# Kernel tuning notes

Hardware: AMD Instinct MI355X
Metric: run time of the kernel (lower is better)

The kernel has to match this reference:

```python
import jax, jax.numpy as jnp
import numpy as np

NEG_SLOPE = 0.2  # PyG GATConv default leaky_relu slope

N_NODES = 50000
N_EDGES = 800000
IN_DIM = 128
HID = 32
HEADS = 4


def setup_inputs() -> dict:
    key = jax.random.key(0)
    ks = jax.random.split(key, 12)
    x = jax.random.normal(ks[0], (N_NODES, IN_DIM), dtype=jnp.float32)
    edge_index = jax.random.randint(ks[1], (2, N_EDGES), 0, N_NODES, dtype=jnp.int64)
    s1 = 1.0 / np.sqrt(IN_DIM)
    s2 = 1.0 / np.sqrt(HID * HEADS)
    return {
        "x": x,
        "edge_index": edge_index,
        # layer 1: GATConv(IN_DIM -> HID, heads=HEADS, concat=True)
        "W1": jax.random.normal(ks[2], (IN_DIM, HEADS * HID), dtype=jnp.float32) * s1,
        "a_src1": jax.random.normal(ks[3], (HEADS, HID), dtype=jnp.float32) * s1,
        "a_dst1": jax.random.normal(ks[4], (HEADS, HID), dtype=jnp.float32) * s1,
        "b1": jnp.zeros((HEADS * HID,), dtype=jnp.float32),
        # head: GATConv(HEADS*HID -> 1, heads=1, concat=False)
        "W2": jax.random.normal(ks[5], (HEADS * HID, 1), dtype=jnp.float32) * s2,
        "a_src2": jax.random.normal(ks[6], (1, 1), dtype=jnp.float32) * s2,
        "a_dst2": jax.random.normal(ks[7], (1, 1), dtype=jnp.float32) * s2,
        "b2": jnp.zeros((1,), dtype=jnp.float32),
    }


def gat_conv(x, src, dst, W, a_src, a_dst, b, heads, out_ch, concat, n_nodes):
    # linear transform -> [N, H, C]
    h = (x @ W).reshape(n_nodes, heads, out_ch)
    # per-node attention halves -> [N, H]
    alpha_s = jnp.einsum('nhc,hc->nh', h, a_src)
    alpha_d = jnp.einsum('nhc,hc->nh', h, a_dst)
    # per-edge logits (gather), leaky relu -> [E, H]
    e = jax.nn.leaky_relu(alpha_s[src] + alpha_d[dst], NEG_SLOPE)
    # segment softmax over destination neighborhoods
    m = jax.ops.segment_max(e, dst, num_segments=n_nodes)  # [N, H]
    m = jnp.where(jnp.isfinite(m), m, 0.0)
    ex = jnp.exp(e - m[dst])
    denom = jax.ops.segment_sum(ex, dst, num_segments=n_nodes)  # [N, H]
    alpha = ex / (denom[dst] + 1e-16)  # [E, H]
    # weighted scatter-aggregate of source messages
    msg = h[src] * alpha[:, :, None]  # [E, H, C]
    out = jax.ops.segment_sum(msg, dst, num_segments=n_nodes)  # [N, H, C]
    out = out.reshape(n_nodes, heads * out_ch) if concat else out.mean(axis=1)
    return out + b


def reference(x, edge_index, W1, a_src1, a_dst1, b1, W2, a_src2, a_dst2, b2):
    n = x.shape[0]
    # PyG GATConv adds self-loops by default
    loops = jnp.arange(n, dtype=edge_index.dtype)
    src = jnp.concatenate([edge_index[0], loops])
    dst = jnp.concatenate([edge_index[1], loops])
    h = gat_conv(x, src, dst, W1, a_src1, a_dst1, b1, HEADS, HID, True, n)
    h = jax.nn.elu(h)  # dropout inactive in eval mode
    out = gat_conv(h, src, dst, W2, a_src2, a_dst2, b2, 1, 1, False, n)
    return out.squeeze(-1)  # [N]
```

## Files before the change

kernel.cpp:

```cpp
#include <hip/hip_runtime.h>
#include <hip/hip_bf16.h>
#include <hip/hip_fp16.h>

#define N_NODES 50000
#define N_EDGES 800000
#define E_TOT   850000
#define GBLK 64
#define GEMM_BLOCKS 782
#define NR 196
#define EPB 4096
#define BIN_BLOCKS 208
#define SEGCAP 8192

__global__ __launch_bounds__(512) void fat_kernel(const float* __restrict__ x,
                                                  const float* __restrict__ W1,
                                                  const float* __restrict__ asrc1,
                                                  const float* __restrict__ adst1,
                                                  __half* __restrict__ h1,
                                                  float* __restrict__ as1,
                                                  float* __restrict__ ad1,
                                                  const int* __restrict__ ei,
                                                  int* __restrict__ rangeCursor,
                                                  unsigned* __restrict__ gseg) {
    __shared__ float xs[32 * 65];
    __shared__ float sredA[8 * 64];
    __shared__ float sredB[8 * 64];
    __shared__ int cnt[NR];
    __shared__ int gbase[NR];

    const int tid = threadIdx.x;

    if (blockIdx.x < BIN_BLOCKS) {
        for (int i = tid; i < NR; i += 512) cnt[i] = 0;
        __syncthreads();

        int e0 = blockIdx.x * EPB + tid * 8;
        bool valid = (e0 < E_TOT);
        int src[8], dst[8], rg[8], rk[8];
        if (valid) {
            if (e0 < N_EDGES) {
                int4 a = *(const int4*)(ei + e0);
                int4 b = *(const int4*)(ei + e0 + 4);
                int4 c = *(const int4*)(ei + N_EDGES + e0);
                int4 d = *(const int4*)(ei + N_EDGES + e0 + 4);
                src[0]=a.x; src[1]=a.y; src[2]=a.z; src[3]=a.w;
                src[4]=b.x; src[5]=b.y; src[6]=b.z; src[7]=b.w;
                dst[0]=c.x; dst[1]=c.y; dst[2]=c.z; dst[3]=c.w;
                dst[4]=d.x; dst[5]=d.y; dst[6]=d.z; dst[7]=d.w;
            } else {
#pragma unroll
                for (int k = 0; k < 8; k++) { src[k] = dst[k] = e0 + k - N_EDGES; }
            }
#pragma unroll
            for (int k = 0; k < 8; k++) {
                rg[k] = dst[k] >> 8;
                rk[k] = atomicAdd(&cnt[rg[k]], 1);
            }
        }
        __syncthreads();
        for (int i = tid; i < NR; i += 512) {
            int c = cnt[i];
            gbase[i] = c ? atomicAdd(&rangeCursor[i], c) : 0;
        }
        __syncthreads();
        if (valid) {
#pragma unroll
            for (int k = 0; k < 8; k++) {
                int pos = gbase[rg[k]] + rk[k];
                if (pos < SEGCAP)
                    gseg[(size_t)rg[k] * SEGCAP + pos] =
                        ((unsigned)(dst[k] & 255) << 17) | (unsigned)src[k];
            }
        }
        return;
    }

    const int lane = tid & 63;
    const int w    = tid >> 6;
    const int head = __builtin_amdgcn_readfirstlane(w >> 1);
    const int ch   = __builtin_amdgcn_readfirstlane(w & 1);
    const int base = (blockIdx.x - BIN_BLOCKS) * GBLK;
    const int node = base + lane;

    const float* __restrict__ wh = W1 + head * 32 + ch * 16;

    float acc[16];
#pragma unroll
    for (int j = 0; j < 16; j++) acc[j] = 0.f;

    for (int kt = 0; kt < 4; kt++) {
        __syncthreads();
        {
            int row = tid >> 3, c4 = tid & 7;
            int n2 = base + row;
            float4 v = make_float4(0.f, 0.f, 0.f, 0.f);
            if (n2 < N_NODES)
                v = *(const float4*)(x + (size_t)n2 * 128 + kt * 32 + c4 * 4);
            xs[(c4 * 4 + 0) * 65 + row] = v.x;
            xs[(c4 * 4 + 1) * 65 + row] = v.y;
            xs[(c4 * 4 + 2) * 65 + row] = v.z;
            xs[(c4 * 4 + 3) * 65 + row] = v.w;
        }
        __syncthreads();

#pragma unroll 4
        for (int kk = 0; kk < 32; kk++) {
            float xv = xs[kk * 65 + lane];
            const float* __restrict__ wr = wh + (size_t)(kt * 32 + kk) * 128;
#pragma unroll
            for (int j = 0; j < 16; j++)
                acc[j] += xv * wr[j];
        }
    }

    if (node < N_NODES) {
        __half2 hp[8];
#pragma unroll
        for (int j = 0; j < 8; j++)
            hp[j] = __floats2half2_rn(acc[2 * j], acc[2 * j + 1]);
        float4* dst = (float4*)(h1 + (size_t)node * 128 + head * 32 + ch * 16);
        dst[0] = ((float4*)hp)[0];
        dst[1] = ((float4*)hp)[1];
    }

    float sa = 0.f, da = 0.f;
#pragma unroll
    for (int j = 0; j < 16; j++) {
        float v = acc[j];
        sa += v * asrc1[head * 32 + ch * 16 + j];
        da += v * adst1[head * 32 + ch * 16 + j];
    }
    sredA[w * 64 + lane] = sa;
    sredB[w * 64 + lane] = da;
    __syncthreads();
    if (tid < 256) {
        int hh = tid >> 6;
        int nd = base + lane;
        if (nd < N_NODES) {
            as1[nd * 4 + hh] = sredA[(hh * 2) * 64 + lane] + sredA[(hh * 2 + 1) * 64 + lane];
            ad1[nd * 4 + hh] = sredB[(hh * 2) * 64 + lane] + sredB[(hh * 2 + 1) * 64 + lane];
        }
    }
}

__global__ __launch_bounds__(512) void finalize_kernel(const int* __restrict__ rangeCursor,
                                                       const unsigned* __restrict__ gseg,
                                                       int* __restrict__ offs,
                                                       int* __restrict__ bucket) {
    __shared__ int rsc[256];
    __shared__ int cnt[256];
    __shared__ int csc[256];
    __shared__ int cur[256];
    __shared__ int lbuf[SEGCAP];

    const int tid = threadIdx.x;
    const int r = blockIdx.x;

    if (tid < 256) rsc[tid] = (tid < NR) ? min(rangeCursor[tid], SEGCAP) : 0;
    __syncthreads();
    for (int d = 1; d < 256; d <<= 1) {
        int u = (tid < 256 && tid >= d) ? rsc[tid - d] : 0;
        __syncthreads();
        if (tid < 256) rsc[tid] += u;
        __syncthreads();
    }
    const int n = min(rangeCursor[r], SEGCAP);
    const int rbase = rsc[r] - n;
    const unsigned* __restrict__ seg = gseg + (size_t)r * SEGCAP;

    if (tid < 256) cnt[tid] = 0;
    __syncthreads();
    for (int i = tid; i < n; i += 512)
        atomicAdd(&cnt[seg[i] >> 17], 1);
    __syncthreads();
    if (tid < 256) csc[tid] = cnt[tid];
    __syncthreads();
    for (int d = 1; d < 256; d <<= 1) {
        int u = (tid < 256 && tid >= d) ? csc[tid - d] : 0;
        __syncthreads();
        if (tid < 256) csc[tid] += u;
        __syncthreads();
    }
    if (tid < 256) {
        int lofs = csc[tid] - cnt[tid];
        cur[tid] = lofs;
        int node = r * 256 + tid;
        if (node < N_NODES) offs[node] = rbase + lofs;
    }
    if (r == NR - 1 && tid == 0) offs[N_NODES] = rbase + n;
    __syncthreads();
    for (int i = tid; i < n; i += 512) {
        unsigned en = seg[i];
        int p = atomicAdd(&cur[en >> 17], 1);
        lbuf[p] = (int)(en & 0x1FFFFu);
    }
    __syncthreads();
    for (int i = tid; i < n; i += 512)
        bucket[rbase + i] = lbuf[i];
}

__global__ __launch_bounds__(256) void agg1_kernel(const __half* __restrict__ h1,
                                                   const float* __restrict__ as1,
                                                   const float* __restrict__ ad1,
                                                   const int* __restrict__ offs,
                                                   const int* __restrict__ bucket,
                                                   const float* __restrict__ b1,
                                                   const float* __restrict__ W2,
                                                   float* __restrict__ h2s) {
    int w = threadIdx.x >> 6, l = threadIdx.x & 63;
    int node = blockIdx.x * 4 + w;
    if (node >= N_NODES) return;
    int sub = l & 15;
    int ep  = l >> 4;
    int head = sub >> 2;
    float adh = ad1[node * 4 + head];
    int a = offs[node];
    int deg = offs[node + 1] - a;

    float c[8];
#pragma unroll
    for (int k = 0; k < 8; k++) c[k] = 0.f;
    float sx = 0.f;

    for (int i = 0; i < deg; i += 4) {
        int idx = i + ep;
        bool valid = idx < deg;
        int s = bucket[a + (valid ? idx : 0)];
        float e = as1[s * 4 + head] + adh;
        e = fmaxf(e, 0.2f * e);
        float ex = valid ? __expf(e) : 0.f;
        float4 hv = *(const float4*)(h1 + (size_t)s * 128 + sub * 8);
        const __half2* hh = (const __half2*)&hv;
        float2 f0 = __half22float2(hh[0]);
        float2 f1 = __half22float2(hh[1]);
        float2 f2 = __half22float2(hh[2]);
        float2 f3 = __half22float2(hh[3]);
        sx += ex;
        c[0] += ex * f0.x; c[1] += ex * f0.y;
        c[2] += ex * f1.x; c[3] += ex * f1.y;
        c[4] += ex * f2.x; c[5] += ex * f2.y;
        c[6] += ex * f3.x; c[7] += ex * f3.y;
    }

#pragma unroll
    for (int k = 0; k < 8; k++) {
        c[k] += __shfl_xor(c[k], 16, 64);
        c[k] += __shfl_xor(c[k], 32, 64);
    }
    sx += __shfl_xor(sx, 16, 64);
    sx += __shfl_xor(sx, 32, 64);

    float r = 1.f / (sx + 1e-16f);
    float4 blo = ((const float4*)b1)[sub * 2];
    float4 bhi = ((const float4*)b1)[sub * 2 + 1];
    float4 wlo = ((const float4*)W2)[sub * 2];
    float4 whi = ((const float4*)W2)[sub * 2 + 1];
    float ob[8] = {blo.x, blo.y, blo.z, blo.w, bhi.x, bhi.y, bhi.z, bhi.w};
    float ow[8] = {wlo.x, wlo.y, wlo.z, wlo.w, whi.x, whi.y, whi.z, whi.w};
    float p = 0.f;
#pragma unroll
    for (int k = 0; k < 8; k++) {
        float o = c[k] * r + ob[k];
        float el = (o > 0.f) ? o : (__expf(o) - 1.f);
        p += el * ow[k];
    }
    p += __shfl_xor(p, 1, 64);
    p += __shfl_xor(p, 2, 64);
    p += __shfl_xor(p, 4, 64);
    p += __shfl_xor(p, 8, 64);
    if (l == 0) h2s[node] = p;
}

__global__ __launch_bounds__(256) void agg2_kernel(const float* __restrict__ h2s,
                                                   const int* __restrict__ offs,
                                                   const int* __restrict__ bucket,
                                                   const float* __restrict__ asrc2,
                                                   const float* __restrict__ adst2,
                                                   const float* __restrict__ b2,
                                                   float* __restrict__ out) {
    int w = threadIdx.x >> 6, l = threadIdx.x & 63;
    int node = blockIdx.x * 4 + w;
    if (node >= N_NODES) return;
    float asc = asrc2[0], adc = adst2[0], bias = b2[0];
    float adn = h2s[node] * adc;
    int a = offs[node], b = offs[node + 1];
    float sx = 0.f, sw = 0.f;
    for (int i = a + l; i < b; i += 64) {
        float hs = h2s[bucket[i]];
        float e = hs * asc + adn;
        e = fmaxf(e, 0.2f * e);
        float ex = __expf(e);
        sx += ex;
        sw += ex * hs;
    }
#pragma unroll
    for (int o = 32; o > 0; o >>= 1) {
        sx += __shfl_xor(sx, o, 64);
        sw += __shfl_xor(sw, o, 64);
    }
    if (l == 0) out[node] = sw / (sx + 1e-16f) + bias;
}


extern "C" void kernel_launch(void* const* d_in, const int* in_sizes, int n_in,
                              void* d_out, int out_size, void* d_ws, size_t ws_size,
                              hipStream_t stream) {
    const float* x     = (const float*)d_in[0];
    const int*   ei    = (const int*)d_in[1];
    const float* W1    = (const float*)d_in[2];
    const float* asrc1 = (const float*)d_in[3];
    const float* adst1 = (const float*)d_in[4];
    const float* b1    = (const float*)d_in[5];
    const float* W2    = (const float*)d_in[6];
    const float* asrc2 = (const float*)d_in[7];
    const float* adst2 = (const float*)d_in[8];
    const float* b2    = (const float*)d_in[9];
    float* out = (float*)d_out;

    char* ws = (char*)d_ws;
    size_t o = 0;
    auto alloc = [&](size_t bytes) -> void* {
        void* p = ws + o;
        o += (bytes + 255) & ~(size_t)255;
        return p;
    };
    int* offs    = (int*)alloc((size_t)(N_NODES + 1) * 4);
    int* bucket  = (int*)alloc((size_t)E_TOT * 4);
    __half* h1   = (__half*)alloc((size_t)N_NODES * 128 * 2);
    float* as1   = (float*)alloc((size_t)N_NODES * 4 * 4);
    float* ad1   = (float*)alloc((size_t)N_NODES * 4 * 4);
    float* h2s   = (float*)alloc((size_t)N_NODES * 4);
    int* rangeCursor = (int*)alloc((size_t)NR * 4);
    unsigned* gseg   = (unsigned*)alloc((size_t)NR * SEGCAP * 4);

    hipMemsetAsync(rangeCursor, 0, (size_t)NR * 4, stream);

    fat_kernel<<<BIN_BLOCKS + GEMM_BLOCKS, 512, 0, stream>>>(
        x, W1, asrc1, adst1, h1, as1, ad1, ei, rangeCursor, gseg);

    finalize_kernel<<<NR, 512, 0, stream>>>(rangeCursor, gseg, offs, bucket);

    agg1_kernel<<<(N_NODES + 3) / 4, 256, 0, stream>>>(
        h1, as1, ad1, offs, bucket, b1, W2, h2s);

    agg2_kernel<<<(N_NODES + 3) / 4, 256, 0, stream>>>(
        h2s, offs, bucket, asrc2, adst2, b2, out);
}
```

Baseline: 102.7 us.

## Move GEMM alongside CSR finalize and widen agg1 per-lane feature slice

The edge-binning pass now runs as its own kernel, and the CSR finalize blocks are merged with the layer-1 GEMM blocks into a single launch that shares a union shared-memory buffer. The GEMM then overlaps with the finalize step instead of with binning, which balances load across the two launches. Separately, agg1 now has each lane handle 16 channels with two float4 loads, so a wavefront processes 8 edges per iteration instead of 4. This doubles the accumulator registers and adds a shuffle stage in exchange for fewer, wider gathers. The merged kernel's shared memory becomes the larger finalize size (about 36KB), which may cut occupancy for the GEMM blocks.

```diff
diff --git a/kernel.cpp b/kernel.cpp
--- a/kernel.cpp
+++ b/kernel.cpp
@@ -12,74 +12,131 @@
 #define BIN_BLOCKS 208
 #define SEGCAP 8192
 
-__global__ __launch_bounds__(512) void fat_kernel(const float* __restrict__ x,
-                                                  const float* __restrict__ W1,
-                                                  const float* __restrict__ asrc1,
-                                                  const float* __restrict__ adst1,
-                                                  __half* __restrict__ h1,
-                                                  float* __restrict__ as1,
-                                                  float* __restrict__ ad1,
-                                                  const int* __restrict__ ei,
+__global__ __launch_bounds__(512) void bin_kernel(const int* __restrict__ ei,
                                                   int* __restrict__ rangeCursor,
                                                   unsigned* __restrict__ gseg) {
-    __shared__ float xs[32 * 65];
-    __shared__ float sredA[8 * 64];
-    __shared__ float sredB[8 * 64];
     __shared__ int cnt[NR];
     __shared__ int gbase[NR];
-
     const int tid = threadIdx.x;
 
-    if (blockIdx.x < BIN_BLOCKS) {
-        for (int i = tid; i < NR; i += 512) cnt[i] = 0;
-        __syncthreads();
-
-        int e0 = blockIdx.x * EPB + tid * 8;
-        bool valid = (e0 < E_TOT);
-        int src[8], dst[8], rg[8], rk[8];
-        if (valid) {
-            if (e0 < N_EDGES) {
-                int4 a = *(const int4*)(ei + e0);
-                int4 b = *(const int4*)(ei + e0 + 4);
-                int4 c = *(const int4*)(ei + N_EDGES + e0);
-                int4 d = *(const int4*)(ei + N_EDGES + e0 + 4);
-                src[0]=a.x; src[1]=a.y; src[2]=a.z; src[3]=a.w;
-                src[4]=b.x; src[5]=b.y; src[6]=b.z; src[7]=b.w;
-                dst[0]=c.x; dst[1]=c.y; dst[2]=c.z; dst[3]=c.w;
-                dst[4]=d.x; dst[5]=d.y; dst[6]=d.z; dst[7]=d.w;
-            } else {
-#pragma unroll
-                for (int k = 0; k < 8; k++) { src[k] = dst[k] = e0 + k - N_EDGES; }
-            }
-#pragma unroll
-            for (int k = 0; k < 8; k++) {
-                rg[k] = dst[k] >> 8;
-                rk[k] = atomicAdd(&cnt[rg[k]], 1);
-            }
-        }
-        __syncthreads();
-        for (int i = tid; i < NR; i += 512) {
-            int c = cnt[i];
-            gbase[i] = c ? atomicAdd(&rangeCursor[i], c) : 0;
-        }
-        __syncthreads();
-        if (valid) {
-#pragma unroll
-            for (int k = 0; k < 8; k++) {
-                int pos = gbase[rg[k]] + rk[k];
-                if (pos < SEGCAP)
-                    gseg[(size_t)rg[k] * SEGCAP + pos] =
-                        ((unsigned)(dst[k] & 255) << 17) | (unsigned)src[k];
-            }
-        }
+    for (int i = tid; i < NR; i += 512) cnt[i] = 0;
+    __syncthreads();
+
+    int e0 = blockIdx.x * EPB + tid * 8;
+    bool valid = (e0 < E_TOT);
+    int src[8], dst[8], rg[8], rk[8];
+    if (valid) {
+        if (e0 < N_EDGES) {
+            int4 a = *(const int4*)(ei + e0);
+            int4 b = *(const int4*)(ei + e0 + 4);
+            int4 c = *(const int4*)(ei + N_EDGES + e0);
+            int4 d = *(const int4*)(ei + N_EDGES + e0 + 4);
+            src[0]=a.x; src[1]=a.y; src[2]=a.z; src[3]=a.w;
+            src[4]=b.x; src[5]=b.y; src[6]=b.z; src[7]=b.w;
+            dst[0]=c.x; dst[1]=c.y; dst[2]=c.z; dst[3]=c.w;
+            dst[4]=d.x; dst[5]=d.y; dst[6]=d.z; dst[7]=d.w;
+        } else {
+#pragma unroll
+            for (int k = 0; k < 8; k++) { src[k] = dst[k] = e0 + k - N_EDGES; }
+        }
+#pragma unroll
+        for (int k = 0; k < 8; k++) {
+            rg[k] = dst[k] >> 8;
+            rk[k] = atomicAdd(&cnt[rg[k]], 1);
+        }
+    }
+    __syncthreads();
+    for (int i = tid; i < NR; i += 512) {
+        int c = cnt[i];
+        gbase[i] = c ? atomicAdd(&rangeCursor[i], c) : 0;
+    }
+    __syncthreads();
+    if (valid) {
+#pragma unroll
+        for (int k = 0; k < 8; k++) {
+            int pos = gbase[rg[k]] + rk[k];
+            if (pos < SEGCAP)
+                gseg[(size_t)rg[k] * SEGCAP + pos] =
+                    ((unsigned)(dst[k] & 255) << 17) | (unsigned)src[k];
+        }
+    }
+}
+
+__global__ __launch_bounds__(512) void fatgf_kernel(const int* __restrict__ rangeCursor,
+                                                    const unsigned* __restrict__ gseg,
+                                                    int* __restrict__ offs,
+                                                    int* __restrict__ bucket,
+                                                    const float* __restrict__ x,
+                                                    const float* __restrict__ W1,
+                                                    const float* __restrict__ asrc1,
+                                                    const float* __restrict__ adst1,
+                                                    __half* __restrict__ h1,
+                                                    float* __restrict__ as1,
+                                                    float* __restrict__ ad1) {
+    __shared__ __align__(16) char smem[(1024 + SEGCAP) * 4];
+    const int tid = threadIdx.x;
+
+    if (blockIdx.x < NR) {
+        int* rsc  = (int*)smem;
+        int* cnt  = rsc + 256;
+        int* csc  = cnt + 256;
+        int* cur  = csc + 256;
+        int* lbuf = cur + 256;
+        const int r = blockIdx.x;
+
+        if (tid < 256) rsc[tid] = (tid < NR) ? min(rangeCursor[tid], SEGCAP) : 0;
+        __syncthreads();
+        for (int d = 1; d < 256; d <<= 1) {
+            int u = (tid < 256 && tid >= d) ? rsc[tid - d] : 0;
+            __syncthreads();
+            if (tid < 256) rsc[tid] += u;
+            __syncthreads();
+        }
+        const int n = min(rangeCursor[r], SEGCAP);
+        const int rbase = rsc[r] - n;
+        const unsigned* __restrict__ seg = gseg + (size_t)r * SEGCAP;
+
+        if (tid < 256) cnt[tid] = 0;
+        __syncthreads();
+        for (int i = tid; i < n; i += 512)
+            atomicAdd(&cnt[seg[i] >> 17], 1);
+        __syncthreads();
+        if (tid < 256) csc[tid] = cnt[tid];
+        __syncthreads();
+        for (int d = 1; d < 256; d <<= 1) {
+            int u = (tid < 256 && tid >= d) ? csc[tid - d] : 0;
+            __syncthreads();
+            if (tid < 256) csc[tid] += u;
+            __syncthreads();
+        }
+        if (tid < 256) {
+            int lofs = csc[tid] - cnt[tid];
+            cur[tid] = lofs;
+            int node = r * 256 + tid;
+            if (node < N_NODES) offs[node] = rbase + lofs;
+        }
+        if (r == NR - 1 && tid == 0) offs[N_NODES] = rbase + n;
+        __syncthreads();
+        for (int i = tid; i < n; i += 512) {
+            unsigned en = seg[i];
+            int p = atomicAdd(&cur[en >> 17], 1);
+            lbuf[p] = (int)(en & 0x1FFFFu);
+        }
+        __syncthreads();
+        for (int i = tid; i < n; i += 512)
+            bucket[rbase + i] = lbuf[i];
         return;
     }
+
+    float* xs    = (float*)smem;
+    float* sredA = xs + 32 * 65;
+    float* sredB = sredA + 8 * 64;
 
     const int lane = tid & 63;
     const int w    = tid >> 6;
     const int head = __builtin_amdgcn_readfirstlane(w >> 1);
     const int ch   = __builtin_amdgcn_readfirstlane(w & 1);
-    const int base = (blockIdx.x - BIN_BLOCKS) * GBLK;
+    const int base = (blockIdx.x - NR) * GBLK;
     const int node = base + lane;
 
     const float* __restrict__ wh = W1 + head * 32 + ch * 16;
@@ -141,62 +198,6 @@
             ad1[nd * 4 + hh] = sredB[(hh * 2) * 64 + lane] + sredB[(hh * 2 + 1) * 64 + lane];
         }
     }
-}
-
-__global__ __launch_bounds__(512) void finalize_kernel(const int* __restrict__ rangeCursor,
-                                                       const unsigned* __restrict__ gseg,
-                                                       int* __restrict__ offs,
-                                                       int* __restrict__ bucket) {
-    __shared__ int rsc[256];
-    __shared__ int cnt[256];
-    __shared__ int csc[256];
-    __shared__ int cur[256];
-    __shared__ int lbuf[SEGCAP];
-
-    const int tid = threadIdx.x;
-    const int r = blockIdx.x;
-
-    if (tid < 256) rsc[tid] = (tid < NR) ? min(rangeCursor[tid], SEGCAP) : 0;
-    __syncthreads();
-    for (int d = 1; d < 256; d <<= 1) {
-        int u = (tid < 256 && tid >= d) ? rsc[tid - d] : 0;
-        __syncthreads();
-        if (tid < 256) rsc[tid] += u;
-        __syncthreads();
-    }
-    const int n = min(rangeCursor[r], SEGCAP);
-    const int rbase = rsc[r] - n;
-    const unsigned* __restrict__ seg = gseg + (size_t)r * SEGCAP;
-
-    if (tid < 256) cnt[tid] = 0;
-    __syncthreads();
-    for (int i = tid; i < n; i += 512)
-        atomicAdd(&cnt[seg[i] >> 17], 1);
-    __syncthreads();
-    if (tid < 256) csc[tid] = cnt[tid];
-    __syncthreads();
-    for (int d = 1; d < 256; d <<= 1) {
-        int u = (tid < 256 && tid >= d) ? csc[tid - d] : 0;
-        __syncthreads();
-        if (tid < 256) csc[tid] += u;
-        __syncthreads();
-    }
-    if (tid < 256) {
-        int lofs = csc[tid] - cnt[tid];
-        cur[tid] = lofs;
-        int node = r * 256 + tid;
-        if (node < N_NODES) offs[node] = rbase + lofs;
-    }
-    if (r == NR - 1 && tid == 0) offs[N_NODES] = rbase + n;
-    __syncthreads();
-    for (int i = tid; i < n; i += 512) {
-        unsigned en = seg[i];
-        int p = atomicAdd(&cur[en >> 17], 1);
-        lbuf[p] = (int)(en & 0x1FFFFu);
-    }
-    __syncthreads();
-    for (int i = tid; i < n; i += 512)
-        bucket[rbase + i] = lbuf[i];
 }
 
 __global__ __launch_bounds__(256) void agg1_kernel(const __half* __restrict__ h1,
@@ -210,64 +211,75 @@
     int w = threadIdx.x >> 6, l = threadIdx.x & 63;
     int node = blockIdx.x * 4 + w;
     if (node >= N_NODES) return;
-    int sub = l & 15;
-    int ep  = l >> 4;
-    int head = sub >> 2;
+    int sub = l & 7;
+    int ep  = l >> 3;
+    int head = sub >> 1;
     float adh = ad1[node * 4 + head];
     int a = offs[node];
     int deg = offs[node + 1] - a;
 
-    float c[8];
-#pragma unroll
-    for (int k = 0; k < 8; k++) c[k] = 0.f;
+    float c[16];
+#pragma unroll
+    for (int k = 0; k < 16; k++) c[k] = 0.f;
     float sx = 0.f;
 
-    for (int i = 0; i < deg; i += 4) {
+    for (int i = 0; i < deg; i += 8) {
         int idx = i + ep;
         bool valid = idx < deg;
         int s = bucket[a + (valid ? idx : 0)];
         float e = as1[s * 4 + head] + adh;
         e = fmaxf(e, 0.2f * e);
         float ex = valid ? __expf(e) : 0.f;
-        float4 hv = *(const float4*)(h1 + (size_t)s * 128 + sub * 8);
-        const __half2* hh = (const __half2*)&hv;
-        float2 f0 = __half22float2(hh[0]);
-        float2 f1 = __half22float2(hh[1]);
-        float2 f2 = __half22float2(hh[2]);
-        float2 f3 = __half22float2(hh[3]);
+        const float4* hp = (const float4*)(h1 + (size_t)s * 128 + sub * 16);
+        float4 hv0 = hp[0];
+        float4 hv1 = hp[1];
+        const __half2* h0 = (const __half2*)&hv0;
+        const __half2* h1p = (const __half2*)&hv1;
         sx += ex;
-        c[0] += ex * f0.x; c[1] += ex * f0.y;
-        c[2] += ex * f1.x; c[3] += ex * f1.y;
-        c[4] += ex * f2.x; c[5] += ex * f2.y;
-        c[6] += ex * f3.x; c[7] += ex * f3.y;
-    }
-
-#pragma unroll
-    for (int k = 0; k < 8; k++) {
+#pragma unroll
+        for (int q = 0; q < 4; q++) {
+            float2 f = __half22float2(h0[q]);
+            c[2 * q]     += ex * f.x;
+            c[2 * q + 1] += ex * f.y;
+        }
+#pragma unroll
+        for (int q = 0; q < 4; q++) {
+            float2 f = __half22float2(h1p[q]);
+            c[8 + 2 * q] += ex * f.x;
+            c[9 + 2 * q] += ex * f.y;
+        }
+    }
+
+#pragma unroll
+    for (int k = 0; k < 16; k++) {
+        c[k] += __shfl_xor(c[k], 8, 64);
         c[k] += __shfl_xor(c[k], 16, 64);
         c[k] += __shfl_xor(c[k], 32, 64);
     }
+    sx += __shfl_xor(sx, 8, 64);
     sx += __shfl_xor(sx, 16, 64);
     sx += __shfl_xor(sx, 32, 64);
 
     float r = 1.f / (sx + 1e-16f);
-    float4 blo = ((const float4*)b1)[sub * 2];
-    float4 bhi = ((const float4*)b1)[sub * 2 + 1];
-    float4 wlo = ((const float4*)W2)[sub * 2];
-    float4 whi = ((const float4*)W2)[sub * 2 + 1];
-    float ob[8] = {blo.x, blo.y, blo.z, blo.w, bhi.x, bhi.y, bhi.z, bhi.w};
-    float ow[8] = {wlo.x, wlo.y, wlo.z, wlo.w, whi.x, whi.y, whi.z, whi.w};
+    const float4* bp = (const float4*)(b1 + sub * 16);
+    const float4* wp = (const float4*)(W2 + sub * 16);
     float p = 0.f;
 #pragma unroll
-    for (int k = 0; k < 8; k++) {
-        float o = c[k] * r + ob[k];
-        float el = (o > 0.f) ? o : (__expf(o) - 1.f);
-        p += el * ow[k];
+    for (int q = 0; q < 4; q++) {
+        float4 bv = bp[q];
+        float4 wv = wp[q];
+        float ob[4] = {bv.x, bv.y, bv.z, bv.w};
+        float ow[4] = {wv.x, wv.y, wv.z, wv.w};
+#pragma unroll
+        for (int t = 0; t < 4; t++) {
+            float o = c[q * 4 + t] * r + ob[t];
+            float el = (o > 0.f) ? o : (__expf(o) - 1.f);
+            p += el * ow[t];
+        }
     }
     p += __shfl_xor(p, 1, 64);
     p += __shfl_xor(p, 2, 64);
     p += __shfl_xor(p, 4, 64);
-    p += __shfl_xor(p, 8, 64);
     if (l == 0) h2s[node] = p;
 }
 
@@ -335,10 +347,11 @@
 
     hipMemsetAsync(rangeCursor, 0, (size_t)NR * 4, stream);
 
-    fat_kernel<<<BIN_BLOCKS + GEMM_BLOCKS, 512, 0, stream>>>(
-        x, W1, asrc1, adst1, h1, as1, ad1, ei, rangeCursor, gseg);
-
-    finalize_kernel<<<NR, 512, 0, stream>>>(rangeCursor, gseg, offs, bucket);
+    bin_kernel<<<BIN_BLOCKS, 512, 0, stream>>>(ei, rangeCursor, gseg);
+
+    fatgf_kernel<<<NR + GEMM_BLOCKS, 512, 0, stream>>>(
+        rangeCursor, gseg, offs, bucket,
+        x, W1, asrc1, adst1, h1, as1, ad1);
 
     agg1_kernel<<<(N_NODES + 3) / 4, 256, 0, stream>>>(
         h1, as1, ad1, offs, bucket, b1, W2, h2s);
```

Result: no change. 103.7 us (+1.0%).

## Pair GEMM with CSR finalize and stage edge logits per wave in agg1

Applied to the files above, without the earlier changes.

The binning pass becomes its own kernel. The GEMM blocks now run alongside the CSR finalize blocks in one fused launch that reuses a shared-memory union, so the dense transform overlaps with the sort instead of with binning. agg1 now loads each chunk of 64 neighbour indices once per wave, computes all four heads' exp logits with one vector load, and stages them in LDS before the gather loop. This removes redundant bucket/as1 loads and exp work, at the cost of extra LDS traffic and a larger shared footprint in the fused kernel, which may lower occupancy of the GEMM blocks.

```diff
diff --git a/kernel.cpp b/kernel.cpp
--- a/kernel.cpp
+++ b/kernel.cpp
@@ -12,74 +12,131 @@
 #define BIN_BLOCKS 208
 #define SEGCAP 8192
 
-__global__ __launch_bounds__(512) void fat_kernel(const float* __restrict__ x,
-                                                  const float* __restrict__ W1,
-                                                  const float* __restrict__ asrc1,
-                                                  const float* __restrict__ adst1,
-                                                  __half* __restrict__ h1,
-                                                  float* __restrict__ as1,
-                                                  float* __restrict__ ad1,
-                                                  const int* __restrict__ ei,
+__global__ __launch_bounds__(512) void bin_kernel(const int* __restrict__ ei,
                                                   int* __restrict__ rangeCursor,
                                                   unsigned* __restrict__ gseg) {
-    __shared__ float xs[32 * 65];
-    __shared__ float sredA[8 * 64];
-    __shared__ float sredB[8 * 64];
     __shared__ int cnt[NR];
     __shared__ int gbase[NR];
-
     const int tid = threadIdx.x;
 
-    if (blockIdx.x < BIN_BLOCKS) {
-        for (int i = tid; i < NR; i += 512) cnt[i] = 0;
-        __syncthreads();
-
-        int e0 = blockIdx.x * EPB + tid * 8;
-        bool valid = (e0 < E_TOT);
-        int src[8], dst[8], rg[8], rk[8];
-        if (valid) {
-            if (e0 < N_EDGES) {
-                int4 a = *(const int4*)(ei + e0);
-                int4 b = *(const int4*)(ei + e0 + 4);
-                int4 c = *(const int4*)(ei + N_EDGES + e0);
-                int4 d = *(const int4*)(ei + N_EDGES + e0 + 4);
-                src[0]=a.x; src[1]=a.y; src[2]=a.z; src[3]=a.w;
-                src[4]=b.x; src[5]=b.y; src[6]=b.z; src[7]=b.w;
-                dst[0]=c.x; dst[1]=c.y; dst[2]=c.z; dst[3]=c.w;
-                dst[4]=d.x; dst[5]=d.y; dst[6]=d.z; dst[7]=d.w;
-            } else {
-#pragma unroll
-                for (int k = 0; k < 8; k++) { src[k] = dst[k] = e0 + k - N_EDGES; }
-            }
-#pragma unroll
-            for (int k = 0; k < 8; k++) {
-                rg[k] = dst[k] >> 8;
-                rk[k] = atomicAdd(&cnt[rg[k]], 1);
-            }
-        }
-        __syncthreads();
-        for (int i = tid; i < NR; i += 512) {
-            int c = cnt[i];
-            gbase[i] = c ? atomicAdd(&rangeCursor[i], c) : 0;
-        }
-        __syncthreads();
-        if (valid) {
-#pragma unroll
-            for (int k = 0; k < 8; k++) {
-                int pos = gbase[rg[k]] + rk[k];
-                if (pos < SEGCAP)
-                    gseg[(size_t)rg[k] * SEGCAP + pos] =
-                        ((unsigned)(dst[k] & 255) << 17) | (unsigned)src[k];
-            }
-        }
+    for (int i = tid; i < NR; i += 512) cnt[i] = 0;
+    __syncthreads();
+
+    int e0 = blockIdx.x * EPB + tid * 8;
+    bool valid = (e0 < E_TOT);
+    int src[8], dst[8], rg[8], rk[8];
+    if (valid) {
+        if (e0 < N_EDGES) {
+            int4 a = *(const int4*)(ei + e0);
+            int4 b = *(const int4*)(ei + e0 + 4);
+            int4 c = *(const int4*)(ei + N_EDGES + e0);
+            int4 d = *(const int4*)(ei + N_EDGES + e0 + 4);
+            src[0]=a.x; src[1]=a.y; src[2]=a.z; src[3]=a.w;
+            src[4]=b.x; src[5]=b.y; src[6]=b.z; src[7]=b.w;
+            dst[0]=c.x; dst[1]=c.y; dst[2]=c.z; dst[3]=c.w;
+            dst[4]=d.x; dst[5]=d.y; dst[6]=d.z; dst[7]=d.w;
+        } else {
+#pragma unroll
+            for (int k = 0; k < 8; k++) { src[k] = dst[k] = e0 + k - N_EDGES; }
+        }
+#pragma unroll
+        for (int k = 0; k < 8; k++) {
+            rg[k] = dst[k] >> 8;
+            rk[k] = atomicAdd(&cnt[rg[k]], 1);
+        }
+    }
+    __syncthreads();
+    for (int i = tid; i < NR; i += 512) {
+        int c = cnt[i];
+        gbase[i] = c ? atomicAdd(&rangeCursor[i], c) : 0;
+    }
+    __syncthreads();
+    if (valid) {
+#pragma unroll
+        for (int k = 0; k < 8; k++) {
+            int pos = gbase[rg[k]] + rk[k];
+            if (pos < SEGCAP)
+                gseg[(size_t)rg[k] * SEGCAP + pos] =
+                    ((unsigned)(dst[k] & 255) << 17) | (unsigned)src[k];
+        }
+    }
+}
+
+__global__ __launch_bounds__(512) void fatgf_kernel(const int* __restrict__ rangeCursor,
+                                                    const unsigned* __restrict__ gseg,
+                                                    int* __restrict__ offs,
+                                                    int* __restrict__ bucket,
+                                                    const float* __restrict__ x,
+                                                    const float* __restrict__ W1,
+                                                    const float* __restrict__ asrc1,
+                                                    const float* __restrict__ adst1,
+                                                    __half* __restrict__ h1,
+                                                    float* __restrict__ as1,
+                                                    float* __restrict__ ad1) {
+    __shared__ __align__(16) char smem[(1024 + SEGCAP) * 4];
+    const int tid = threadIdx.x;
+
+    if (blockIdx.x < NR) {
+        int* rsc  = (int*)smem;
+        int* cnt  = rsc + 256;
+        int* csc  = cnt + 256;
+        int* cur  = csc + 256;
+        int* lbuf = cur + 256;
+        const int r = blockIdx.x;
+
+        if (tid < 256) rsc[tid] = (tid < NR) ? min(rangeCursor[tid], SEGCAP) : 0;
+        __syncthreads();
+        for (int d = 1; d < 256; d <<= 1) {
+            int u = (tid < 256 && tid >= d) ? rsc[tid - d] : 0;
+            __syncthreads();
+            if (tid < 256) rsc[tid] += u;
+            __syncthreads();
+        }
+        const int n = min(rangeCursor[r], SEGCAP);
+        const int rbase = rsc[r] - n;
+        const unsigned* __restrict__ seg = gseg + (size_t)r * SEGCAP;
+
+        if (tid < 256) cnt[tid] = 0;
+        __syncthreads();
+        for (int i = tid; i < n; i += 512)
+            atomicAdd(&cnt[seg[i] >> 17], 1);
+        __syncthreads();
+        if (tid < 256) csc[tid] = cnt[tid];
+        __syncthreads();
+        for (int d = 1; d < 256; d <<= 1) {
+            int u = (tid < 256 && tid >= d) ? csc[tid - d] : 0;
+            __syncthreads();
+            if (tid < 256) csc[tid] += u;
+            __syncthreads();
+        }
+        if (tid < 256) {
+            int lofs = csc[tid] - cnt[tid];
+            cur[tid] = lofs;
+            int node = r * 256 + tid;
+            if (node < N_NODES) offs[node] = rbase + lofs;
+        }
+        if (r == NR - 1 && tid == 0) offs[N_NODES] = rbase + n;
+        __syncthreads();
+        for (int i = tid; i < n; i += 512) {
+            unsigned en = seg[i];
+            int p = atomicAdd(&cur[en >> 17], 1);
+            lbuf[p] = (int)(en & 0x1FFFFu);
+        }
+        __syncthreads();
+        for (int i = tid; i < n; i += 512)
+            bucket[rbase + i] = lbuf[i];
         return;
     }
+
+    float* xs    = (float*)smem;
+    float* sredA = xs + 32 * 65;
+    float* sredB = sredA + 8 * 64;
 
     const int lane = tid & 63;
     const int w    = tid >> 6;
     const int head = __builtin_amdgcn_readfirstlane(w >> 1);
     const int ch   = __builtin_amdgcn_readfirstlane(w & 1);
-    const int base = (blockIdx.x - BIN_BLOCKS) * GBLK;
+    const int base = (blockIdx.x - NR) * GBLK;
     const int node = base + lane;
 
     const float* __restrict__ wh = W1 + head * 32 + ch * 16;
@@ -143,62 +200,6 @@
     }
 }
 
-__global__ __launch_bounds__(512) void finalize_kernel(const int* __restrict__ rangeCursor,
-                                                       const unsigned* __restrict__ gseg,
-                                                       int* __restrict__ offs,
-                                                       int* __restrict__ bucket) {
-    __shared__ int rsc[256];
-    __shared__ int cnt[256];
-    __shared__ int csc[256];
-    __shared__ int cur[256];
-    __shared__ int lbuf[SEGCAP];
-
-    const int tid = threadIdx.x;
-    const int r = blockIdx.x;
-
-    if (tid < 256) rsc[tid] = (tid < NR) ? min(rangeCursor[tid], SEGCAP) : 0;
-    __syncthreads();
-    for (int d = 1; d < 256; d <<= 1) {
-        int u = (tid < 256 && tid >= d) ? rsc[tid - d] : 0;
-        __syncthreads();
-        if (tid < 256) rsc[tid] += u;
-        __syncthreads();
-    }
-    const int n = min(rangeCursor[r], SEGCAP);
-    const int rbase = rsc[r] - n;
-    const unsigned* __restrict__ seg = gseg + (size_t)r * SEGCAP;
-
-    if (tid < 256) cnt[tid] = 0;
-    __syncthreads();
-    for (int i = tid; i < n; i += 512)
-        atomicAdd(&cnt[seg[i] >> 17], 1);
-    __syncthreads();
-    if (tid < 256) csc[tid] = cnt[tid];
-    __syncthreads();
-    for (int d = 1; d < 256; d <<= 1) {
-        int u = (tid < 256 && tid >= d) ? csc[tid - d] : 0;
-        __syncthreads();
-        if (tid < 256) csc[tid] += u;
-        __syncthreads();
-    }
-    if (tid < 256) {
-        int lofs = csc[tid] - cnt[tid];
-        cur[tid] = lofs;
-        int node = r * 256 + tid;
-        if (node < N_NODES) offs[node] = rbase + lofs;
-    }
-    if (r == NR - 1 && tid == 0) offs[N_NODES] = rbase + n;
-    __syncthreads();
-    for (int i = tid; i < n; i += 512) {
-        unsigned en = seg[i];
-        int p = atomicAdd(&cur[en >> 17], 1);
-        lbuf[p] = (int)(en & 0x1FFFFu);
-    }
-    __syncthreads();
-    for (int i = tid; i < n; i += 512)
-        bucket[rbase + i] = lbuf[i];
-}
-
 __global__ __launch_bounds__(256) void agg1_kernel(const __half* __restrict__ h1,
                                                    const float* __restrict__ as1,
                                                    const float* __restrict__ ad1,
@@ -207,39 +208,65 @@
                                                    const float* __restrict__ b1,
                                                    const float* __restrict__ W2,
                                                    float* __restrict__ h2s) {
+    __shared__ int   sbuf[4][64];
+    __shared__ float exbuf[4][64][4];
+
     int w = threadIdx.x >> 6, l = threadIdx.x & 63;
     int node = blockIdx.x * 4 + w;
     if (node >= N_NODES) return;
     int sub = l & 15;
     int ep  = l >> 4;
     int head = sub >> 2;
-    float adh = ad1[node * 4 + head];
     int a = offs[node];
     int deg = offs[node + 1] - a;
+    float4 adv = *(const float4*)(ad1 + (size_t)node * 4);
 
     float c[8];
 #pragma unroll
     for (int k = 0; k < 8; k++) c[k] = 0.f;
     float sx = 0.f;
 
-    for (int i = 0; i < deg; i += 4) {
-        int idx = i + ep;
-        bool valid = idx < deg;
-        int s = bucket[a + (valid ? idx : 0)];
-        float e = as1[s * 4 + head] + adh;
-        e = fmaxf(e, 0.2f * e);
-        float ex = valid ? __expf(e) : 0.f;
-        float4 hv = *(const float4*)(h1 + (size_t)s * 128 + sub * 8);
-        const __half2* hh = (const __half2*)&hv;
-        float2 f0 = __half22float2(hh[0]);
-        float2 f1 = __half22float2(hh[1]);
-        float2 f2 = __half22float2(hh[2]);
-        float2 f3 = __half22float2(hh[3]);
-        sx += ex;
-        c[0] += ex * f0.x; c[1] += ex * f0.y;
-        c[2] += ex * f1.x; c[3] += ex * f1.y;
-        c[4] += ex * f2.x; c[5] += ex * f2.y;
-        c[6] += ex * f3.x; c[7] += ex * f3.y;
+    for (int base = 0; base < deg; base += 64) {
+        int cd = min(deg - base, 64);
+        {
+            bool v = l < cd;
+            int s = bucket[a + base + (v ? l : 0)];
+            sbuf[w][l] = s;
+            float4 asv = *(const float4*)(as1 + (size_t)s * 4);
+            float e0 = asv.x + adv.x, e1 = asv.y + adv.y;
+            float e2 = asv.z + adv.z, e3 = asv.w + adv.w;
+            e0 = fmaxf(e0, 0.2f * e0);
+            e1 = fmaxf(e1, 0.2f * e1);
+            e2 = fmaxf(e2, 0.2f * e2);
+            e3 = fmaxf(e3, 0.2f * e3);
+            float4 exv;
+            exv.x = v ? __expf(e0) : 0.f;
+            exv.y = v ? __expf(e1) : 0.f;
+            exv.z = v ? __expf(e2) : 0.f;
+            exv.w = v ? __expf(e3) : 0.f;
+            *(float4*)&exbuf[w][l][0] = exv;
+        }
+        __builtin_amdgcn_wave_barrier();
+        for (int g = 0; g < cd; g += 4) {
+            int j = g + ep;
+            bool v2 = j < cd;
+            int jj = v2 ? j : 0;
+            int s = sbuf[w][jj];
+            float ex = exbuf[w][jj][head];
+            if (!v2) ex = 0.f;
+            float4 hv = *(const float4*)(h1 + (size_t)s * 128 + sub * 8);
+            const __half2* hh = (const __half2*)&hv;
+            float2 f0 = __half22float2(hh[0]);
+            float2 f1 = __half22float2(hh[1]);
+            float2 f2 = __half22float2(hh[2]);
+            float2 f3 = __half22float2(hh[3]);
+            sx += ex;
+            c[0] += ex * f0.x; c[1] += ex * f0.y;
+            c[2] += ex * f1.x; c[3] += ex * f1.y;
+            c[4] += ex * f2.x; c[5] += ex * f2.y;
+            c[6] += ex * f3.x; c[7] += ex * f3.y;
+        }
+        __builtin_amdgcn_wave_barrier();
     }
 
 #pragma unroll
@@ -335,10 +362,11 @@
 
     hipMemsetAsync(rangeCursor, 0, (size_t)NR * 4, stream);
 
-    fat_kernel<<<BIN_BLOCKS + GEMM_BLOCKS, 512, 0, stream>>>(
-        x, W1, asrc1, adst1, h1, as1, ad1, ei, rangeCursor, gseg);
-
-    finalize_kernel<<<NR, 512, 0, stream>>>(rangeCursor, gseg, offs, bucket);
+    bin_kernel<<<BIN_BLOCKS, 512, 0, stream>>>(ei, rangeCursor, gseg);
+
+    fatgf_kernel<<<NR + GEMM_BLOCKS, 512, 0, stream>>>(
+        rangeCursor, gseg, offs, bucket,
+        x, W1, asrc1, adst1, h1, as1, ad1);
 
     agg1_kernel<<<(N_NODES + 3) / 4, 256, 0, stream>>>(
         h1, as1, ad1, offs, bucket, b1, W2, h2s);
```

After: 99.04 us. 3.6% less time.
